# Optimization experiments

Hardware: AMD Instinct MI355X
Metric: run time of the kernel (lower is better)

## Reference

```python
import jax, jax.numpy as jnp
import numpy as np

DIM = 512
CODEBOOK_SIZE = 8192
B, N = 8, 2048
EPS = 1e-12


def setup_inputs() -> dict:
    key = jax.random.key(0)
    k1, k2, k3 = jax.random.split(key, 3)
    x = jax.random.normal(k1, (B, N, DIM), dtype=jnp.float32)
    # matches torch.randn(codebook_size, dim) * dim ** -0.5
    codebook = jax.random.normal(k2, (CODEBOOK_SIZE, DIM), dtype=jnp.float32) * DIM ** -0.5
    # nn.Linear(dim, dim, bias=False) weight, applied as x @ W.T
    W = jax.random.normal(k3, (DIM, DIM), dtype=jnp.float32) * DIM ** -0.5
    return {"x": x, "codebook": codebook, "W": W}


def _l2norm(t):
    return t / jnp.maximum(jnp.linalg.norm(t, axis=-1, keepdims=True), EPS)


def _rotate_from_to(q, x):
    """Rotation trick: forward value == q, gradient flows through x via a
    detached Householder-style rotation (R = I - 2ww^T + 2 q_hat x_hat^T)
    and detached norm rescaling."""
    sg = jax.lax.stop_gradient
    norm_x = jnp.linalg.norm(x, axis=-1, keepdims=True)
    norm_q = jnp.linalg.norm(q, axis=-1, keepdims=True)
    x_hat = x / jnp.maximum(norm_x, EPS)
    q_hat = q / jnp.maximum(norm_q, EPS)
    w = sg(_l2norm(x_hat + q_hat))
    x_hat_d, q_hat_d = sg(x_hat), sg(q_hat)
    e = x
    rotated = (e
               - 2.0 * jnp.sum(e * w, axis=-1, keepdims=True) * w
               + 2.0 * jnp.sum(e * x_hat_d, axis=-1, keepdims=True) * q_hat_d)
    return rotated * sg(norm_q / jnp.maximum(norm_x, EPS))


def reference(x, codebook, W):
    # implicit codebook = Linear(codebook)
    codes = jnp.einsum('cd,ed->ce', codebook, W)  # [C, d]
    d2 = -2.0 * jnp.einsum('bnd,cd->bnc', x, codes) + jnp.sum(codes * codes, axis=-1)
    indices = jnp.argmin(jax.lax.stop_gradient(d2), axis=-1)  # [b, n] int
    quantized = codes[indices]  # gather -> [b, n, d]
    commit_loss = jnp.mean((jax.lax.stop_gradient(x) - quantized) ** 2)
    quantized = _rotate_from_to(quantized, x)
    return quantized, indices, commit_loss
```

## Files before the change

### kernel.cpp

```cpp
#include <hip/hip_runtime.h>


#define DIMK  512
#define CBN   8192
#define MROWS 16384

#define SX 24.0f
#define SC 500.0f
#define INV_SS (1.0f / (SX * SC))
#define DELTA 0.3f
#define DKEY  1231
#define NSLOT 3

#define WS_CODES   0UL
#define WS_XQ      16777216UL
#define WS_CQ      25165824UL
#define WS_NORMS   29360128UL
#define WS_CAND    29392896UL
#define WS_CBH     29392896UL
#define WS_CBL     37781504UL
#define WS_WH      54558720UL
#define WS_WL      55083008UL
#define WS_LOSSP   55607296UL

typedef short s16x8 __attribute__((ext_vector_type(8)));
typedef int   i32x4 __attribute__((ext_vector_type(4)));
typedef float f32x4 __attribute__((ext_vector_type(4)));

__device__ __forceinline__ unsigned short f2bf(float f) {
    unsigned u = __float_as_uint(f);
    unsigned r = u + 0x7FFFu + ((u >> 16) & 1u);
    return (unsigned short)(r >> 16);
}
__device__ __forceinline__ float bf2f(unsigned short h) {
    return __uint_as_float(((unsigned)h) << 16);
}
__device__ __forceinline__ void load_lds16(const void* g, void* l) {
    __builtin_amdgcn_global_load_lds((const __attribute__((address_space(1))) void*)g,
                                     (__attribute__((address_space(3))) void*)l,
                                     16, 0, 0);
}
__device__ __forceinline__ signed char q8(float v, float s) {
    return (signed char)__float2int_rn(fminf(fmaxf(v * s, -127.0f), 127.0f));
}
__device__ __forceinline__ unsigned packSlot(float d, unsigned col) {
    int k = (int)((d + 16.0f) * 4096.0f);
    k = k < 0 ? 0 : (k > 524287 ? 524287 : k);
    return ((unsigned)k << 13) | col;
}

__global__ __launch_bounds__(256) void split_bf16(const float* __restrict__ in,
                                                  unsigned short* __restrict__ hi,
                                                  unsigned short* __restrict__ lo,
                                                  int n4) {
    int i = blockIdx.x * 256 + threadIdx.x;
    if (i >= n4) return;
    float4 v = ((const float4*)in)[i];
    ushort4 h, l;
    h.x = f2bf(v.x); l.x = f2bf(v.x - bf2f(h.x));
    h.y = f2bf(v.y); l.y = f2bf(v.y - bf2f(h.y));
    h.z = f2bf(v.z); l.z = f2bf(v.z - bf2f(h.z));
    h.w = f2bf(v.w); l.w = f2bf(v.w - bf2f(h.w));
    ((ushort4*)hi)[i] = h;
    ((ushort4*)lo)[i] = l;
}

__global__ __launch_bounds__(256) void quant_x(const float* __restrict__ in,
                                               signed char* __restrict__ out, int n4) {
    int i = blockIdx.x * 256 + threadIdx.x;
    if (i >= n4) return;
    float4 v = ((const float4*)in)[i];
    char4 c;
    c.x = q8(v.x, SX); c.y = q8(v.y, SX); c.z = q8(v.z, SX); c.w = q8(v.w, SX);
    ((char4*)out)[i] = c;
}

__global__ __launch_bounds__(256) void codes_mfma(
        const unsigned short* __restrict__ Ah_g, const unsigned short* __restrict__ Al_g,
        const unsigned short* __restrict__ Bh_g, const unsigned short* __restrict__ Bl_g,
        float* __restrict__ C, signed char* __restrict__ Cq, float* __restrict__ Norms) {
    __shared__ __align__(16) unsigned short Ahi[128 * 32];
    __shared__ __align__(16) unsigned short Alo[128 * 32];
    __shared__ __align__(16) unsigned short Bhi[128 * 32];
    __shared__ __align__(16) unsigned short Blo[128 * 32];

    const int t    = threadIdx.x;
    const int w    = t >> 6;
    const int lane = t & 63;
    const int quad = lane >> 4;
    const int l16  = lane & 15;
    const int wm   = w & 1, wn = w >> 1;
    const int rowBase = blockIdx.x * 128;
    const int colBase = blockIdx.y * 128;

    f32x4 acc[4][4];
    #pragma unroll
    for (int i = 0; i < 4; ++i)
        #pragma unroll
        for (int j = 0; j < 4; ++j)
            acc[i][j] = (f32x4)(0.0f);

    const int mr = t >> 2;
    const int kq = (t & 3) * 8;
    const size_t gxa = (size_t)(rowBase + mr) * DIMK + kq;
    const size_t gxb = gxa + (size_t)64 * DIMK;
    const size_t gca = (size_t)(colBase + mr) * DIMK + kq;
    const size_t gcb = gca + (size_t)64 * DIMK;
    const int l0 = w * 512;
    const int l1 = 2048 + w * 512;

    for (int k0 = 0; k0 < DIMK; k0 += 32) {
        load_lds16(Ah_g + gxa + k0, &Ahi[l0]);
        load_lds16(Ah_g + gxb + k0, &Ahi[l1]);
        load_lds16(Al_g + gxa + k0, &Alo[l0]);
        load_lds16(Al_g + gxb + k0, &Alo[l1]);
        load_lds16(Bh_g + gca + k0, &Bhi[l0]);
        load_lds16(Bh_g + gcb + k0, &Bhi[l1]);
        load_lds16(Bl_g + gca + k0, &Blo[l0]);
        load_lds16(Bl_g + gcb + k0, &Blo[l1]);
        __syncthreads();

        s16x8 ah[4], al[4], bh[4], bl[4];
        #pragma unroll
        for (int i = 0; i < 4; ++i) {
            const int m = wm * 64 + i * 16 + l16;
            ah[i] = *(const s16x8*)&Ahi[m * 32 + quad * 8];
            al[i] = *(const s16x8*)&Alo[m * 32 + quad * 8];
        }
        #pragma unroll
        for (int j = 0; j < 4; ++j) {
            const int n = wn * 64 + j * 16 + l16;
            bh[j] = *(const s16x8*)&Bhi[n * 32 + quad * 8];
            bl[j] = *(const s16x8*)&Blo[n * 32 + quad * 8];
        }
        #pragma unroll
        for (int i = 0; i < 4; ++i)
            #pragma unroll
            for (int j = 0; j < 4; ++j) {
                acc[i][j] = __builtin_amdgcn_mfma_f32_16x16x32_bf16(ah[i], bh[j], acc[i][j], 0, 0, 0);
                acc[i][j] = __builtin_amdgcn_mfma_f32_16x16x32_bf16(ah[i], bl[j], acc[i][j], 0, 0, 0);
                acc[i][j] = __builtin_amdgcn_mfma_f32_16x16x32_bf16(al[i], bh[j], acc[i][j], 0, 0, 0);
            }
        __syncthreads();
    }

    #pragma unroll
    for (int i = 0; i < 4; ++i) {
        #pragma unroll
        for (int r = 0; r < 4; ++r) {
            const int row = rowBase + wm * 64 + i * 16 + quad * 4 + r;
            float nsum = 0.0f;
            #pragma unroll
            for (int j = 0; j < 4; ++j) {
                const int col = colBase + wn * 64 + j * 16 + l16;
                const float v = acc[i][j][r];
                C[(size_t)row * DIMK + col] = v;
                Cq[(size_t)row * DIMK + col] = q8(v, SC);
                nsum = fmaf(v, v, nsum);
            }
            nsum += __shfl_xor(nsum, 1, 64);
            nsum += __shfl_xor(nsum, 2, 64);
            nsum += __shfl_xor(nsum, 4, 64);
            nsum += __shfl_xor(nsum, 8, 64);
            if (l16 == 0) atomicAdd(&Norms[row], nsum);
        }
    }
}

__global__ __launch_bounds__(512) void d2_argmin_i8(
        const signed char* __restrict__ Xq,
        const signed char* __restrict__ Cq,
        const float* __restrict__ Norms,
        unsigned* __restrict__ Cand) {
    __shared__ __align__(16) signed char Ash[128 * 64];
    __shared__ __align__(16) signed char Bsh[128 * 64];

    const int t    = threadIdx.x;
    const int w    = t >> 6;
    const int lane = t & 63;
    const int quad = lane >> 4;
    const int l16  = lane & 15;
    const int wm   = w & 3, wn = w >> 2;
    const int rowBase = blockIdx.x * 128;
    const int colBase = blockIdx.y * 128;

    i32x4 acc[2][4];
    #pragma unroll
    for (int i = 0; i < 2; ++i)
        #pragma unroll
        for (int j = 0; j < 4; ++j)
            acc[i][j] = (i32x4)(0);

    const int mr = t >> 2;
    const int kc = (t & 3) * 16;
    const size_t gxa = (size_t)(rowBase + mr) * DIMK + kc;
    const size_t gca = (size_t)(colBase + mr) * DIMK + kc;
    const int lb = w * 1024;

    for (int k0 = 0; k0 < DIMK; k0 += 64) {
        load_lds16(Xq + gxa + k0, &Ash[lb]);
        load_lds16(Cq + gca + k0, &Bsh[lb]);
        __syncthreads();

        i32x4 af[2], bf[4];
        #pragma unroll
        for (int i = 0; i < 2; ++i)
            af[i] = *(const i32x4*)&Ash[(wm * 32 + i * 16 + l16) * 64 + quad * 16];
        #pragma unroll
        for (int j = 0; j < 4; ++j)
            bf[j] = *(const i32x4*)&Bsh[(wn * 64 + j * 16 + l16) * 64 + quad * 16];
        #pragma unroll
        for (int i = 0; i < 2; ++i)
            #pragma unroll
            for (int j = 0; j < 4; ++j)
                acc[i][j] = __builtin_amdgcn_mfma_i32_16x16x64_i8(af[i], bf[j], acc[i][j], 0, 0, 0);
        __syncthreads();
    }

    float nrm[4];
    #pragma unroll
    for (int j = 0; j < 4; ++j)
        nrm[j] = Norms[colBase + wn * 64 + j * 16 + l16];

    const int subtile = blockIdx.y * 2 + wn;
    const unsigned long long qmask = 0xFFFFull << (quad * 16);
    const unsigned long long ltm = (lane == 0) ? 0ull : (~0ull >> (64 - lane));
    const unsigned colG = colBase + wn * 64 + l16;

    #pragma unroll
    for (int i = 0; i < 2; ++i) {
        #pragma unroll
        for (int r = 0; r < 4; ++r) {
            float d0 = fmaf((float)acc[i][0][r], -2.0f * INV_SS, nrm[0]);
            float d1 = fmaf((float)acc[i][1][r], -2.0f * INV_SS, nrm[1]);
            float d2v = fmaf((float)acc[i][2][r], -2.0f * INV_SS, nrm[2]);
            float d3 = fmaf((float)acc[i][3][r], -2.0f * INV_SS, nrm[3]);
            float mn = fminf(fminf(d0, d1), fminf(d2v, d3));
            mn = fminf(mn, __shfl_xor(mn, 1, 64));
            mn = fminf(mn, __shfl_xor(mn, 2, 64));
            mn = fminf(mn, __shfl_xor(mn, 4, 64));
            mn = fminf(mn, __shfl_xor(mn, 8, 64));
            const float thr = mn + DELTA;
            unsigned long long b0 = __ballot(d0 <= thr);
            unsigned long long b1 = __ballot(d1 <= thr);
            unsigned long long b2 = __ballot(d2v <= thr);
            unsigned long long b3 = __ballot(d3 <= thr);
            const int row = rowBase + wm * 32 + i * 16 + quad * 4 + r;
            unsigned* slot = Cand + ((size_t)row * 128 + subtile) * NSLOT;
            if (d0 <= thr) {
                int rk = __popcll(b0 & qmask & ltm);
                if (rk < NSLOT) slot[rk] = packSlot(d0, colG + 0);
            }
            if (d1 <= thr) {
                int rk = __popcll(b0 & qmask) + __popcll(b1 & qmask & ltm);
                if (rk < NSLOT) slot[rk] = packSlot(d1, colG + 16);
            }
            if (d2v <= thr) {
                int rk = __popcll(b0 & qmask) + __popcll(b1 & qmask)
                       + __popcll(b2 & qmask & ltm);
                if (rk < NSLOT) slot[rk] = packSlot(d2v, colG + 32);
            }
            if (d3 <= thr) {
                int rk = __popcll(b0 & qmask) + __popcll(b1 & qmask)
                       + __popcll(b2 & qmask) + __popcll(b3 & qmask & ltm);
                if (rk < NSLOT) slot[rk] = packSlot(d3, colG + 48);
            }
        }
    }
}

__global__ __launch_bounds__(256) void refine_gather(
        const float* __restrict__ X, const float* __restrict__ Codes,
        const float* __restrict__ Norms, const unsigned* __restrict__ Cand,
        float* __restrict__ outQ, float* __restrict__ outIdx,
        float* __restrict__ lossP) {
    const int t    = threadIdx.x;
    const int w    = t >> 6;
    const int lane = t & 63;
    const int row  = blockIdx.x * 4 + w;

    const unsigned* cp = Cand + (size_t)row * 128 * NSLOT + lane * 6;
    unsigned sl[6];
    #pragma unroll
    for (int s = 0; s < 6; ++s) sl[s] = cp[s];

    unsigned mn = sl[0];
    #pragma unroll
    for (int s = 1; s < 6; ++s) mn = min(mn, sl[s]);
    #pragma unroll
    for (int mask = 1; mask < 64; mask <<= 1)
        mn = min(mn, (unsigned)__shfl((int)mn, lane ^ mask, 64));
    const unsigned thrp = (((mn >> 13) + DKEY) << 13) | 0x1FFFu;

    const float4 xa = *(const float4*)(X + (size_t)row * DIMK + lane * 8);
    const float4 xb = *(const float4*)(X + (size_t)row * DIMK + lane * 8 + 4);

    float bestD = __builtin_inff();
    unsigned bestIdx = 0xFFFFFFFFu;

    #pragma unroll
    for (int s = 0; s < 6; ++s) {
        unsigned long long bm = __ballot(sl[s] <= thrp);
        while (bm) {
            const int src = __ffsll(bm) - 1;
            bm &= bm - 1;
            const unsigned sv = (unsigned)__shfl((int)sl[s], src, 64);
            const unsigned idx = sv & 0x1FFFu;
            const float4 ca = *(const float4*)(Codes + (size_t)idx * DIMK + lane * 8);
            const float4 cbv = *(const float4*)(Codes + (size_t)idx * DIMK + lane * 8 + 4);
            float s2 = xa.x * ca.x + xa.y * ca.y + xa.z * ca.z + xa.w * ca.w
                     + xb.x * cbv.x + xb.y * cbv.y + xb.z * cbv.z + xb.w * cbv.w;
            #pragma unroll
            for (int mm = 1; mm < 64; mm <<= 1) s2 += __shfl_xor(s2, mm, 64);
            const float d2 = fmaf(-2.0f, s2, Norms[idx]);
            if (d2 < bestD || (d2 == bestD && idx < bestIdx)) { bestD = d2; bestIdx = idx; }
        }
    }

    const float4 qa = *(const float4*)(Codes + (size_t)bestIdx * DIMK + lane * 8);
    const float4 qb = *(const float4*)(Codes + (size_t)bestIdx * DIMK + lane * 8 + 4);
    *(float4*)(outQ + (size_t)row * DIMK + lane * 8) = qa;
    *(float4*)(outQ + (size_t)row * DIMK + lane * 8 + 4) = qb;
    float dx0 = xa.x - qa.x, dx1 = xa.y - qa.y, dx2 = xa.z - qa.z, dx3 = xa.w - qa.w;
    float dy0 = xb.x - qb.x, dy1 = xb.y - qb.y, dy2 = xb.z - qb.z, dy3 = xb.w - qb.w;
    float s = dx0 * dx0 + dx1 * dx1 + dx2 * dx2 + dx3 * dx3
            + dy0 * dy0 + dy1 * dy1 + dy2 * dy2 + dy3 * dy3;
    #pragma unroll
    for (int off = 32; off > 0; off >>= 1) s += __shfl_down(s, off);
    if (lane == 0) {
        lossP[row] = s;
        outIdx[row] = (float)bestIdx;
    }
}

__global__ __launch_bounds__(256) void finalize_loss(const float* __restrict__ lossPartials,
                                                     float* __restrict__ outLoss) {
    const int t = threadIdx.x;
    float s = 0.0f;
    for (int i = t; i < MROWS; i += 256) s += lossPartials[i];
    #pragma unroll
    for (int off = 32; off > 0; off >>= 1) s += __shfl_down(s, off);
    __shared__ float red[4];
    if ((t & 63) == 0) red[t >> 6] = s;
    __syncthreads();
    if (t == 0)
        *outLoss = (red[0] + red[1] + red[2] + red[3]) * (1.0f / (float)((size_t)MROWS * DIMK));
}

extern "C" void kernel_launch(void* const* d_in, const int* in_sizes, int n_in,
                              void* d_out, int out_size, void* d_ws, size_t ws_size,
                              hipStream_t stream) {
    const float* x  = (const float*)d_in[0];
    const float* cb = (const float*)d_in[1];
    const float* W  = (const float*)d_in[2];
    float* out = (float*)d_out;

    char* ws = (char*)d_ws;
    float* codes          = (float*)(ws + WS_CODES);
    signed char* xq       = (signed char*)(ws + WS_XQ);
    signed char* cq       = (signed char*)(ws + WS_CQ);
    float* norms          = (float*)(ws + WS_NORMS);
    unsigned* cand        = (unsigned*)(ws + WS_CAND);
    unsigned short* cbh   = (unsigned short*)(ws + WS_CBH);
    unsigned short* cbl   = (unsigned short*)(ws + WS_CBL);
    unsigned short* wh    = (unsigned short*)(ws + WS_WH);
    unsigned short* wl    = (unsigned short*)(ws + WS_WL);
    float* lossP          = (float*)(ws + WS_LOSSP);

    hipMemsetAsync(norms, 0, CBN * 4, stream);

    split_bf16<<<(CBN * DIMK / 4 + 255) / 256, 256, 0, stream>>>(cb, cbh, cbl, CBN * DIMK / 4);
    split_bf16<<<(DIMK * DIMK / 4 + 255) / 256, 256, 0, stream>>>(W, wh, wl, DIMK * DIMK / 4);
    quant_x<<<(MROWS * DIMK / 4 + 255) / 256, 256, 0, stream>>>(x, xq, MROWS * DIMK / 4);

    codes_mfma<<<dim3(CBN / 128, DIMK / 128), 256, 0, stream>>>(cbh, cbl, wh, wl, codes, cq, norms);

    hipMemsetAsync(cand, 0xFF, (size_t)MROWS * 128 * NSLOT * 4, stream);

    d2_argmin_i8<<<dim3(MROWS / 128, CBN / 128), 512, 0, stream>>>(xq, cq, norms, cand);

    refine_gather<<<MROWS / 4, 256, 0, stream>>>(x, codes, norms, cand, out,
                                                 out + (size_t)MROWS * DIMK, lossP);
    finalize_loss<<<1, 256, 0, stream>>>(lossP, out + (size_t)MROWS * DIMK + MROWS);
}
```

Measured before the change: 295.4 us.

## Swizzle LDS layouts and enlarge per-wave tiles in int8 distance GEMM

Applies an XOR swizzle to the LDS write and read offsets in both the bf16 codes GEMM and the int8 distance GEMM, to cut LDS bank conflicts on fragment reads. The int8 argmin kernel also drops from 8 waves to 4 waves per block, so each wave computes a 64x64 tile (4x4 MFMA fragments) instead of 32x64. That gives more register-level reuse of the B fragments and fewer LDS reads per MFMA, in exchange for more accumulator registers and possibly lower occupancy (launch bounds 256,3).

```diff
diff --git a/kernel.cpp b/kernel.cpp
--- a/kernel.cpp
+++ b/kernel.cpp
@@ -101,13 +101,15 @@
             acc[i][j] = (f32x4)(0.0f);
 
     const int mr = t >> 2;
-    const int kq = (t & 3) * 8;
+    const int kq = ((t & 3) ^ ((t >> 3) & 3)) * 8;
     const size_t gxa = (size_t)(rowBase + mr) * DIMK + kq;
     const size_t gxb = gxa + (size_t)64 * DIMK;
     const size_t gca = (size_t)(colBase + mr) * DIMK + kq;
     const size_t gcb = gca + (size_t)64 * DIMK;
     const int l0 = w * 512;
     const int l1 = 2048 + w * 512;
+
+    const int swz8 = (quad ^ ((l16 >> 1) & 3)) * 8;
 
     for (int k0 = 0; k0 < DIMK; k0 += 32) {
         load_lds16(Ah_g + gxa + k0, &Ahi[l0]);
@@ -124,14 +126,14 @@
         #pragma unroll
         for (int i = 0; i < 4; ++i) {
             const int m = wm * 64 + i * 16 + l16;
-            ah[i] = *(const s16x8*)&Ahi[m * 32 + quad * 8];
-            al[i] = *(const s16x8*)&Alo[m * 32 + quad * 8];
+            ah[i] = *(const s16x8*)&Ahi[m * 32 + swz8];
+            al[i] = *(const s16x8*)&Alo[m * 32 + swz8];
         }
         #pragma unroll
         for (int j = 0; j < 4; ++j) {
             const int n = wn * 64 + j * 16 + l16;
-            bh[j] = *(const s16x8*)&Bhi[n * 32 + quad * 8];
-            bl[j] = *(const s16x8*)&Blo[n * 32 + quad * 8];
+            bh[j] = *(const s16x8*)&Bhi[n * 32 + swz8];
+            bl[j] = *(const s16x8*)&Blo[n * 32 + swz8];
         }
         #pragma unroll
         for (int i = 0; i < 4; ++i)
@@ -167,7 +169,7 @@
     }
 }
 
-__global__ __launch_bounds__(512) void d2_argmin_i8(
+__global__ __launch_bounds__(256, 3) void d2_argmin_i8(
         const signed char* __restrict__ Xq,
         const signed char* __restrict__ Cq,
         const float* __restrict__ Norms,
@@ -180,40 +182,48 @@
     const int lane = t & 63;
     const int quad = lane >> 4;
     const int l16  = lane & 15;
-    const int wm   = w & 3, wn = w >> 2;
+    const int wm   = w & 1, wn = w >> 1;
     const int rowBase = blockIdx.x * 128;
     const int colBase = blockIdx.y * 128;
 
-    i32x4 acc[2][4];
-    #pragma unroll
-    for (int i = 0; i < 2; ++i)
+    i32x4 acc[4][4];
+    #pragma unroll
+    for (int i = 0; i < 4; ++i)
         #pragma unroll
         for (int j = 0; j < 4; ++j)
             acc[i][j] = (i32x4)(0);
 
-    const int mr = t >> 2;
-    const int kc = (t & 3) * 16;
-    const size_t gxa = (size_t)(rowBase + mr) * DIMK + kc;
-    const size_t gca = (size_t)(colBase + mr) * DIMK + kc;
-    const int lb = w * 1024;
+    const int mr  = t >> 2;
+    const int kcs = ((t & 3) ^ ((t >> 3) & 3)) * 16;
+    const size_t gxa = (size_t)(rowBase + mr) * DIMK + kcs;
+    const size_t gxb = gxa + (size_t)64 * DIMK;
+    const size_t gca = (size_t)(colBase + mr) * DIMK + kcs;
+    const size_t gcb = gca + (size_t)64 * DIMK;
+    const int l0 = w * 1024;
+    const int l1 = 4096 + w * 1024;
+
+    const int swz  = (quad ^ ((l16 >> 1) & 3)) * 16;
+    const int aoff = (wm * 64 + l16) * 64 + swz;
+    const int boff = (wn * 64 + l16) * 64 + swz;
 
     for (int k0 = 0; k0 < DIMK; k0 += 64) {
-        load_lds16(Xq + gxa + k0, &Ash[lb]);
-        load_lds16(Cq + gca + k0, &Bsh[lb]);
+        load_lds16(Xq + gxa + k0, &Ash[l0]);
+        load_lds16(Xq + gxb + k0, &Ash[l1]);
+        load_lds16(Cq + gca + k0, &Bsh[l0]);
+        load_lds16(Cq + gcb + k0, &Bsh[l1]);
         __syncthreads();
 
-        i32x4 af[2], bf[4];
-        #pragma unroll
-        for (int i = 0; i < 2; ++i)
-            af[i] = *(const i32x4*)&Ash[(wm * 32 + i * 16 + l16) * 64 + quad * 16];
-        #pragma unroll
-        for (int j = 0; j < 4; ++j)
-            bf[j] = *(const i32x4*)&Bsh[(wn * 64 + j * 16 + l16) * 64 + quad * 16];
-        #pragma unroll
-        for (int i = 0; i < 2; ++i)
+        i32x4 af[4];
+        #pragma unroll
+        for (int i = 0; i < 4; ++i)
+            af[i] = *(const i32x4*)&Ash[aoff + i * 1024];
+        #pragma unroll
+        for (int j = 0; j < 4; ++j) {
+            const i32x4 bfj = *(const i32x4*)&Bsh[boff + j * 1024];
             #pragma unroll
-            for (int j = 0; j < 4; ++j)
-                acc[i][j] = __builtin_amdgcn_mfma_i32_16x16x64_i8(af[i], bf[j], acc[i][j], 0, 0, 0);
+            for (int i = 0; i < 4; ++i)
+                acc[i][j] = __builtin_amdgcn_mfma_i32_16x16x64_i8(af[i], bfj, acc[i][j], 0, 0, 0);
+        }
         __syncthreads();
     }
 
@@ -228,7 +238,7 @@
     const unsigned colG = colBase + wn * 64 + l16;
 
     #pragma unroll
-    for (int i = 0; i < 2; ++i) {
+    for (int i = 0; i < 4; ++i) {
         #pragma unroll
         for (int r = 0; r < 4; ++r) {
             float d0 = fmaf((float)acc[i][0][r], -2.0f * INV_SS, nrm[0]);
@@ -245,7 +255,7 @@
             unsigned long long b1 = __ballot(d1 <= thr);
             unsigned long long b2 = __ballot(d2v <= thr);
             unsigned long long b3 = __ballot(d3 <= thr);
-            const int row = rowBase + wm * 32 + i * 16 + quad * 4 + r;
+            const int row = rowBase + wm * 64 + i * 16 + quad * 4 + r;
             unsigned* slot = Cand + ((size_t)row * 128 + subtile) * NSLOT;
             if (d0 <= thr) {
                 int rk = __popcll(b0 & qmask & ltm);
@@ -377,7 +387,7 @@
 
     hipMemsetAsync(cand, 0xFF, (size_t)MROWS * 128 * NSLOT * 4, stream);
 
-    d2_argmin_i8<<<dim3(MROWS / 128, CBN / 128), 512, 0, stream>>>(xq, cq, norms, cand);
+    d2_argmin_i8<<<dim3(MROWS / 128, CBN / 128), 256, 0, stream>>>(xq, cq, norms, cand);
 
     refine_gather<<<MROWS / 4, 256, 0, stream>>>(x, codes, norms, cand, out,
                                                  out + (size_t)MROWS * DIMK, lossP);
```

New measurement: 315.4 us. 6.8% more time.
